# Optimization experiments

Hardware: AMD Instinct MI355X
Metric: run time of the kernel (lower is better)

## Reference

```python
import math
import jax, jax.numpy as jnp
import numpy as np

HEAD_NUM = 8
DIM = 512
D_K = DIM // HEAD_NUM  # 64
M_FEAT = 256
B, L = 4, 2048
STAB = 1e-5


def _orthogonal_gaussian(m, d, rng):
    num_squares = m // d
    blocks = []
    for _ in range(num_squares):
        q, _ = np.linalg.qr(rng.standard_normal((d, d)))
        blocks.append(q.T)
    rem = m - d * num_squares
    if rem:
        q, _ = np.linalg.qr(rng.standard_normal((d, d)))
        blocks.append(q.T[:rem])
    mat = np.concatenate(blocks, axis=0)
    mat = mat / math.sqrt(num_squares + rem / d)
    return mat.astype(np.float32)


def setup_inputs() -> dict:
    key = jax.random.key(0)
    ks = jax.random.split(key, 12)
    rng = np.random.default_rng(0)
    inp = {
        'query': jax.random.normal(ks[0], (B, L, DIM), jnp.float32),
        'key': jax.random.normal(ks[1], (B, L, DIM), jnp.float32),
        'value': jax.random.normal(ks[2], (B, L, DIM), jnp.float32),
        'proj': jnp.asarray(_orthogonal_gaussian(M_FEAT, D_K, rng)),  # [M, d_k]
        'w_q_w': jax.random.normal(ks[3], (DIM, DIM), jnp.float32) * 0.02,
        'w_q_b': jnp.zeros((DIM,), jnp.float32),
        'w_k_w': jax.random.normal(ks[4], (DIM, DIM), jnp.float32) * 0.02,
        'w_k_b': jnp.zeros((DIM,), jnp.float32),
        'w_v_w': jax.random.normal(ks[5], (DIM, DIM), jnp.float32) * 0.02,
        'w_v_b': jnp.zeros((DIM,), jnp.float32),
        'w_o_w': jax.random.normal(ks[6], (DIM, DIM), jnp.float32) * 0.02,
        'w_o_b': jnp.zeros((DIM,), jnp.float32),
    }
    return inp


def _relu_kernel(data, proj):
    # data: [B,L,H,D], proj: [M,D] -> [B,L,H,M]
    ratio = 1.0 / math.sqrt(proj.shape[0])
    return jax.nn.relu(ratio * jnp.einsum('blhd,md->blhm', data, proj)) + STAB


def _favor_causal(qp, kp, vs):
    # qp, kp: [L,B,H,M]; vs: [L,B,H,D] -> num [L,B,H,D], den [L,B,H]
    b, h, m = qp.shape[1], qp.shape[2], qp.shape[3]
    d = vs.shape[3]
    carry0 = (jnp.zeros((b, h, m, d), qp.dtype), jnp.zeros((b, h, m), qp.dtype))

    def step(carry, inp):
        s_kv, s_k = carry
        q_l, k_l, v_l = inp
        s_kv = s_kv + jnp.einsum('bhm,bhd->bhmd', k_l, v_l)
        s_k = s_k + k_l
        num = jnp.einsum('bhmd,bhm->bhd', s_kv, q_l)
        den = jnp.sum(q_l * s_k, axis=-1)
        return (s_kv, s_k), (num, den)

    _, (num, den) = jax.lax.scan(step, carry0, (qp, kp, vs))
    return num, den


def reference(query, key, value, proj, w_q_w, w_q_b, w_k_w, w_k_b, w_v_w, w_v_b, w_o_w, w_o_b):
    bsz = query.shape[0]
    q = (query @ w_q_w.T + w_q_b).reshape(bsz, -1, HEAD_NUM, D_K)
    k = (key @ w_k_w.T + w_k_b).reshape(bsz, -1, HEAD_NUM, D_K)
    v = (value @ w_v_w.T + w_v_b).reshape(bsz, -1, HEAD_NUM, D_K)
    qp = jnp.swapaxes(_relu_kernel(q, proj), 0, 1)  # [L,B,H,M]
    kp = jnp.swapaxes(_relu_kernel(k, proj), 0, 1)
    vs = jnp.swapaxes(v, 0, 1)                      # [L,B,H,D]
    num, den = _favor_causal(qp, kp, vs)
    attn = jnp.swapaxes(num, 0, 1) / jnp.swapaxes(den, 0, 1)[..., None]  # [B,L,H,D]
    attn = attn.reshape(bsz, -1, HEAD_NUM * D_K)
    return attn @ w_o_w.T + w_o_b
```

## Files before the change

kernel.cpp:

```cpp
#include <hip/hip_runtime.h>
#include <stdint.h>

#define B_ 4
#define L_ 2048
#define H_ 8
#define DK 64
#define M_ 256
#define DIM_ 512
#define NTOK (B_ * L_)
#define CHK 128
#define NC (L_ / CHK)
#define BH (B_ * H_)
#define RATIO 0.0625f
#define STABC 1e-5f

typedef unsigned short ushort_t;
typedef __attribute__((ext_vector_type(8))) short bf8v;
typedef __attribute__((ext_vector_type(4))) float f4v;

#define MFMA16(a, b, c) __builtin_amdgcn_mfma_f32_16x16x32_bf16(a, b, c, 0, 0, 0)

__device__ __forceinline__ ushort_t f2bf(float f) {
  uint32_t u = __float_as_uint(f);
  return (ushort_t)((u + 0x7fffu + ((u >> 16) & 1u)) >> 16);
}
__device__ __forceinline__ float bf2f(ushort_t u) { return __uint_as_float(((uint32_t)u) << 16); }

__device__ __forceinline__ void gll16(const void* g, void* l) {
  __builtin_amdgcn_global_load_lds((const __attribute__((address_space(1))) void*)g,
                                   (__attribute__((address_space(3))) void*)l, 16, 0, 0);
}

__device__ __forceinline__ bf8v ldfrag(const ushort_t* base, int row, int cb) {
  return *(const bf8v*)((const char*)base + row * 128 + (cb ^ ((row & 7) << 4)));
}
__device__ __forceinline__ bf8v ldfrag256(const ushort_t* base, int row, int cb) {
  return *(const bf8v*)((const char*)base + row * 256 + (cb ^ ((row & 7) << 4)));
}
__device__ __forceinline__ bf8v ldfrag512(const ushort_t* base, int row, int cb) {
  return *(const bf8v*)((const char*)base + row * 512 + (cb ^ ((row & 7) << 4)));
}

__global__ __launch_bounds__(256) void cvt_w(const float* __restrict__ wq, const float* __restrict__ wk,
                                             const float* __restrict__ wv, const float* __restrict__ wo,
                                             const float* __restrict__ pj, ushort_t* __restrict__ d) {
  int i = (blockIdx.x * 256 + threadIdx.x) * 8;
  const float* s;
  int off;
  if (i < 262144)       { s = wq; off = i; }
  else if (i < 524288)  { s = wk; off = i - 262144; }
  else if (i < 786432)  { s = wv; off = i - 524288; }
  else if (i < 1048576) { s = wo; off = i - 786432; }
  else                  { s = pj; off = i - 1048576; }
  float4 a = *(const float4*)(s + off);
  float4 b = *(const float4*)(s + off + 4);
  union { ushort_t u[8]; uint4 vv; } o;
  o.u[0] = f2bf(a.x); o.u[1] = f2bf(a.y); o.u[2] = f2bf(a.z); o.u[3] = f2bf(a.w);
  o.u[4] = f2bf(b.x); o.u[5] = f2bf(b.y); o.u[6] = f2bf(b.z); o.u[7] = f2bf(b.w);
  *(uint4*)(d + i) = o.vv;
}

__global__ __launch_bounds__(256) void qkvgemm_k(const float* __restrict__ q, const float* __restrict__ k,
                                                 const float* __restrict__ v, const ushort_t* __restrict__ Wc,
                                                 const float* __restrict__ bq, const float* __restrict__ bk,
                                                 const float* __restrict__ bv, ushort_t* __restrict__ XHq,
                                                 ushort_t* __restrict__ XHk, ushort_t* __restrict__ VT) {
  __shared__ char SB[65536];
  ushort_t* Tt = (ushort_t*)SB;
  const int z = blockIdx.z;
  const float* X = (z == 0) ? q : (z == 1) ? k : v;
  const ushort_t* Bw = Wc + (size_t)z * 262144;
  const float* bias = (z == 0) ? bq : (z == 1) ? bk : bv;
  const int tid = threadIdx.x, lane = tid & 63, w = tid >> 6;
  const int bm = blockIdx.x * 128, bn = blockIdx.y * 128;
  const int srow = w * 8 + (lane >> 3);
  const int scol = (((lane & 7) * 16) ^ ((lane >> 3) << 4)) >> 1;
  const int wr = (w >> 1) * 64, wc = (w & 1) * 64;
  const int fr = lane & 15, ks = lane >> 4, fq = lane >> 4;
  f4v acc[4][4] = {};
  {
#pragma unroll
    for (int i = 0; i < 4; ++i)
      gll16(Bw + (size_t)(bn + i * 32 + srow) * DIM_ + scol, SB + 32768 + i * 4096 + w * 1024);
#pragma unroll
    for (int i = 0; i < 4; ++i) {
      int e = tid + i * 256;
      int r = e >> 3, g = e & 7;
      const float* src = X + (size_t)(bm + r) * DIM_ + g * 8;
      float4 f0 = *(const float4*)src;
      float4 f1 = *(const float4*)(src + 4);
      union { ushort_t u[8]; bf8v v8; } pk;
      pk.u[0] = f2bf(f0.x); pk.u[1] = f2bf(f0.y); pk.u[2] = f2bf(f0.z); pk.u[3] = f2bf(f0.w);
      pk.u[4] = f2bf(f1.x); pk.u[5] = f2bf(f1.y); pk.u[6] = f2bf(f1.z); pk.u[7] = f2bf(f1.w);
      *(bf8v*)(SB + r * 128 + ((g * 16) ^ ((r & 7) << 4))) = pk.v8;
    }
  }
  __syncthreads();
  for (int t = 0; t < 8; ++t) {
    const ushort_t* curA = (const ushort_t*)(SB + (t & 1) * 16384);
    const ushort_t* curB = (const ushort_t*)(SB + 32768 + (t & 1) * 16384);
    char* nxtA = SB + ((t + 1) & 1) * 16384;
    char* nxtB = SB + 32768 + ((t + 1) & 1) * 16384;
    const int nk = (t + 1) * 64;
    float4 fA[4][2];
    if (t < 7) {
#pragma unroll
      for (int i = 0; i < 4; ++i) {
        int e = tid + i * 256;
        int r = e >> 3, g = e & 7;
        const float* src = X + (size_t)(bm + r) * DIM_ + nk + g * 8;
        fA[i][0] = *(const float4*)src;
        fA[i][1] = *(const float4*)(src + 4);
      }
#pragma unroll
      for (int i = 0; i < 4; ++i)
        gll16(Bw + (size_t)(bn + i * 32 + srow) * DIM_ + nk + scol, nxtB + i * 4096 + w * 1024);
    }
#pragma unroll
    for (int kk = 0; kk < 2; ++kk) {
      const int cb = kk * 64 + ks * 16;
      bf8v av[4], bv2[4];
#pragma unroll
      for (int m = 0; m < 4; ++m) av[m] = ldfrag(curA, wr + m * 16 + fr, cb);
#pragma unroll
      for (int n = 0; n < 4; ++n) bv2[n] = ldfrag(curB, wc + n * 16 + fr, cb);
#pragma unroll
      for (int m = 0; m < 4; ++m)
#pragma unroll
        for (int n = 0; n < 4; ++n) acc[m][n] = MFMA16(av[m], bv2[n], acc[m][n]);
    }
    if (t < 7) {
#pragma unroll
      for (int i = 0; i < 4; ++i) {
        int e = tid + i * 256;
        int r = e >> 3, g = e & 7;
        union { ushort_t u[8]; bf8v v8; } pk;
        pk.u[0] = f2bf(fA[i][0].x); pk.u[1] = f2bf(fA[i][0].y);
        pk.u[2] = f2bf(fA[i][0].z); pk.u[3] = f2bf(fA[i][0].w);
        pk.u[4] = f2bf(fA[i][1].x); pk.u[5] = f2bf(fA[i][1].y);
        pk.u[6] = f2bf(fA[i][1].z); pk.u[7] = f2bf(fA[i][1].w);
        *(bf8v*)(nxtA + r * 128 + ((g * 16) ^ ((r & 7) << 4))) = pk.v8;
      }
    }
    __syncthreads();
  }
  if (z == 2) {
#pragma unroll
    for (int m = 0; m < 4; ++m)
#pragma unroll
      for (int n = 0; n < 4; ++n) {
        int cl = wc + n * 16 + fr;
        float bsv = bias[bn + cl];
#pragma unroll
        for (int j = 0; j < 4; ++j) {
          int rl = wr + m * 16 + fq * 4 + j;
          Tt[cl * 136 + rl] = f2bf(acc[m][n][j] + bsv);
        }
      }
    __syncthreads();
    const int dl = tid >> 1, seg = tid & 1;
    const int c = bn + dl;
    const int bh2 = (bm >> 11) * 8 + (c >> 6);
    const int drow = c & 63;
    size_t vbase = ((size_t)(bh2 * 64 + drow)) * L_ + (bm & 2047) + seg * 64;
#pragma unroll
    for (int qq = 0; qq < 8; ++qq)
      *(uint4*)&VT[vbase + qq * 8] = *(const uint4*)&Tt[dl * 136 + seg * 64 + qq * 8];
  } else {
    ushort_t* Y = (z == 0) ? XHq : XHk;
#pragma unroll
    for (int m = 0; m < 4; ++m)
#pragma unroll
      for (int n = 0; n < 4; ++n) {
        int col = bn + wc + n * 16 + fr;
        float bsv = bias[col];
#pragma unroll
        for (int j = 0; j < 4; ++j) {
          int row = bm + wr + m * 16 + fq * 4 + j;
          Y[(size_t)row * DIM_ + col] = f2bf(acc[m][n][j] + bsv);
        }
      }
  }
}

__global__ __launch_bounds__(256) void cp2_k(const ushort_t* __restrict__ XHk, const ushort_t* __restrict__ P,
                                             const ushort_t* __restrict__ VT, ushort_t* __restrict__ kp,
                                             ushort_t* __restrict__ S) {
  __shared__ ushort_t Ps[256 * 64];
  __shared__ ushort_t Xs[128 * 64];
  __shared__ ushort_t Kt[256 * 128];
  const int ci = blockIdx.x, bh = blockIdx.y;
  const int b = bh >> 3, h = bh & 7;
  const int tid = threadIdx.x, lane = tid & 63, w = tid >> 6;
  const int srow = w * 8 + (lane >> 3);
  const int scol = (((lane & 7) * 16) ^ ((lane >> 3) << 4)) >> 1;
  const int fr = lane & 15, ks = lane >> 4, fq = lane >> 4;
  const int l0 = ci * CHK;
#pragma unroll
  for (int i = 0; i < 8; ++i)
    gll16(P + (size_t)(i * 32 + srow) * 64 + scol, (char*)Ps + i * 4096 + w * 1024);
#pragma unroll
  for (int i = 0; i < 4; ++i)
    gll16(XHk + (size_t)(b * L_ + l0 + i * 32 + srow) * DIM_ + h * 64 + scol, (char*)Xs + i * 4096 + w * 1024);
  __syncthreads();
  {
    f4v acc[4][8] = {};
#pragma unroll
    for (int kk = 0; kk < 2; ++kk) {
      const int cb = kk * 64 + ks * 16;
      bf8v av[4], bv[8];
#pragma unroll
      for (int m = 0; m < 4; ++m) av[m] = ldfrag(Ps, w * 64 + m * 16 + fr, cb);
#pragma unroll
      for (int n = 0; n < 8; ++n) bv[n] = ldfrag(Xs, n * 16 + fr, cb);
#pragma unroll
      for (int m = 0; m < 4; ++m)
#pragma unroll
        for (int n = 0; n < 8; ++n) acc[m][n] = MFMA16(av[m], bv[n], acc[m][n]);
    }
#pragma unroll
    for (int m = 0; m < 4; ++m)
#pragma unroll
      for (int n = 0; n < 8; ++n) {
        const int mb = w * 64 + m * 16 + fq * 4;
        const int ll = n * 16 + fr;
        ushort_t bvv[4];
#pragma unroll
        for (int j = 0; j < 4; ++j) {
          float v = fmaxf(RATIO * acc[m][n][j], 0.f) + STABC;
          bvv[j] = f2bf(v);
          *(ushort_t*)((char*)Kt + (mb + j) * 256 + ((ll * 2) ^ (((mb + j) & 7) << 4))) = bvv[j];
        }
        uint2 pk;
        pk.x = (uint32_t)bvv[0] | ((uint32_t)bvv[1] << 16);
        pk.y = (uint32_t)bvv[2] | ((uint32_t)bvv[3] << 16);
        *(uint2*)(kp + ((size_t)bh * L_ + l0 + ll) * M_ + mb) = pk;
      }
  }
  __syncthreads();
  f4v accS[5][4] = {};
  for (int kt = 0; kt < 2; ++kt) {
#pragma unroll
    for (int i = 0; i < 2; ++i)
      gll16(VT + ((size_t)bh * 64 + i * 32 + srow) * L_ + l0 + kt * 64 + scol, (char*)Xs + i * 4096 + w * 1024);
    if (tid < 32) ((uint32_t*)Xs)[2048 + tid] = 0x3f803f80u;
    __syncthreads();
#pragma unroll
    for (int kk = 0; kk < 2; ++kk) {
      const int cbA = kk * 64 + ks * 16;
      const int cbK = kt * 128 + kk * 64 + ks * 16;
      bf8v av[5], bv[4];
#pragma unroll
      for (int a = 0; a < 5; ++a) av[a] = ldfrag(Xs, a * 16 + fr, cbA);
#pragma unroll
      for (int n = 0; n < 4; ++n) bv[n] = ldfrag256(Kt, w * 64 + n * 16 + fr, cbK);
#pragma unroll
      for (int a = 0; a < 5; ++a)
#pragma unroll
        for (int n = 0; n < 4; ++n) accS[a][n] = MFMA16(av[a], bv[n], accS[a][n]);
    }
    __syncthreads();
  }
  const size_t base = ((size_t)bh * NC + ci) * 65;
#pragma unroll
  for (int a = 0; a < 5; ++a)
#pragma unroll
    for (int n = 0; n < 4; ++n)
#pragma unroll
      for (int j = 0; j < 4; ++j) {
        int row = a * 16 + fq * 4 + j;
        if (row < 65) S[(base + row) * M_ + w * 64 + n * 16 + fr] = f2bf(accS[a][n][j]);
      }
}

__global__ __launch_bounds__(256) void prefix2_k(ushort_t* __restrict__ S) {
  const int g = blockIdx.x * 256 + threadIdx.x;
  const int bh = g / 2080, r = g - bh * 2080;
  ushort_t* base = S + (size_t)bh * (NC * 65 * M_) + (size_t)r * 8;
  uint4 v[16];
#pragma unroll
  for (int ci = 0; ci < NC; ++ci) v[ci] = *(const uint4*)(base + (size_t)ci * (65 * M_));
  float c[8] = {};
#pragma unroll
  for (int ci = 0; ci < NC; ++ci) {
    union { uint4 u; ushort_t s[8]; } in, out;
    in.u = v[ci];
#pragma unroll
    for (int e = 0; e < 8; ++e) {
      float t = bf2f(in.s[e]);
      out.s[e] = f2bf(c[e]);
      c[e] += t;
    }
    *(uint4*)(base + (size_t)ci * (65 * M_)) = out.u;
  }
}

__global__ __launch_bounds__(512) void qkout3_k(const ushort_t* __restrict__ XHq, const ushort_t* __restrict__ P,
                                                const ushort_t* __restrict__ kp, const ushort_t* __restrict__ VT,
                                                const ushort_t* __restrict__ S, ushort_t* __restrict__ attn) {
  __shared__ char LB[114688];
  ushort_t* Qp = (ushort_t*)LB;
  ushort_t* R1 = (ushort_t*)(LB + 65536);
  ushort_t* R2 = (ushort_t*)(LB + 98304);
  const int ci = blockIdx.x, bh = blockIdx.y;
  const int b = bh >> 3, h = bh & 7;
  const int tid = threadIdx.x, lane = tid & 63, w = tid >> 6;
  const int srow = w * 8 + (lane >> 3);
  const int scol = (((lane & 7) * 16) ^ ((lane >> 3) << 4)) >> 1;
  const int fr = lane & 15, ks = lane >> 4, fq = lane >> 4;
  const int l0 = ci * CHK;
  const size_t rowb = (size_t)bh * L_ + l0;
  const size_t tokb = (size_t)b * L_ + l0;
  const size_t sbase = ((size_t)bh * NC + ci) * 65;
#pragma unroll
  for (int i = 0; i < 4; ++i)
    gll16(P + (size_t)(i * 64 + srow) * 64 + scol, (char*)R1 + i * 8192 + w * 1024);
#pragma unroll
  for (int i = 0; i < 2; ++i)
    gll16(XHq + (tokb + i * 64 + srow) * DIM_ + h * 64 + scol, (char*)R2 + i * 8192 + w * 1024);
  __syncthreads();
  {
    f4v accF[2][8] = {};
#pragma unroll
    for (int kk = 0; kk < 2; ++kk) {
      const int cb = kk * 64 + ks * 16;
      bf8v av[2], bv[8];
#pragma unroll
      for (int m = 0; m < 2; ++m) av[m] = ldfrag(R1, w * 32 + m * 16 + fr, cb);
#pragma unroll
      for (int n = 0; n < 8; ++n) bv[n] = ldfrag(R2, n * 16 + fr, cb);
#pragma unroll
      for (int m = 0; m < 2; ++m)
#pragma unroll
        for (int n = 0; n < 8; ++n) accF[m][n] = MFMA16(av[m], bv[n], accF[m][n]);
    }
#pragma unroll
    for (int m = 0; m < 2; ++m)
#pragma unroll
      for (int n = 0; n < 8; ++n) {
        const int mb = w * 32 + m * 16 + fq * 4;
        const int ll = n * 16 + fr;
        ushort_t bvv[4];
#pragma unroll
        for (int j = 0; j < 4; ++j)
          bvv[j] = f2bf(fmaxf(RATIO * accF[m][n][j], 0.f) + STABC);
        uint2 pk;
        pk.x = (uint32_t)bvv[0] | ((uint32_t)bvv[1] << 16);
        pk.y = (uint32_t)bvv[2] | ((uint32_t)bvv[3] << 16);
        *(uint2*)((char*)Qp + ll * 512 + ((mb * 2) ^ ((ll & 7) << 4))) = pk;
      }
  }
  __syncthreads();
  const int qr = (w & 3) * 32, qc = (w >> 2) * 64;
  const int orow = w * 16;
  f4v accA[2][4] = {};
  f4v acc2[5] = {};
  for (int kt = 0; kt < 4; ++kt) {
#pragma unroll
    for (int i = 0; i < 2; ++i)
      gll16(kp + (rowb + i * 64 + srow) * M_ + kt * 64 + scol, (char*)R1 + i * 8192 + w * 1024);
    gll16(S + (sbase + srow) * M_ + kt * 64 + scol, (char*)R2 + w * 1024);
    if (tid < 32)
      ((uint32_t*)R2)[2048 + tid] = ((const uint32_t*)(S + (sbase + 64) * M_ + kt * 64))[tid];
    __syncthreads();
#pragma unroll
    for (int kk = 0; kk < 2; ++kk) {
      const int cb = kk * 64 + ks * 16;
      const int cbQ = kt * 128 + cb;
      bf8v aq[2], bk_[4], a2, sv[5];
#pragma unroll
      for (int m = 0; m < 2; ++m) aq[m] = ldfrag512(Qp, qr + m * 16 + fr, cbQ);
#pragma unroll
      for (int n = 0; n < 4; ++n) bk_[n] = ldfrag(R1, qc + n * 16 + fr, cb);
#pragma unroll
      for (int m = 0; m < 2; ++m)
#pragma unroll
        for (int n = 0; n < 4; ++n) accA[m][n] = MFMA16(aq[m], bk_[n], accA[m][n]);
      a2 = ldfrag512(Qp, orow + fr, cbQ);
#pragma unroll
      for (int n = 0; n < 5; ++n) sv[n] = ldfrag(R2, n * 16 + fr, cb);
#pragma unroll
      for (int n = 0; n < 5; ++n) acc2[n] = MFMA16(a2, sv[n], acc2[n]);
    }
    __syncthreads();
  }
#pragma unroll
  for (int m = 0; m < 2; ++m)
#pragma unroll
    for (int n = 0; n < 4; ++n)
#pragma unroll
      for (int j = 0; j < 4; ++j) {
        int row = qr + m * 16 + fq * 4 + j;
        int col = qc + n * 16 + fr;
        float v = (col <= row) ? accA[m][n][j] : 0.f;
        *(ushort_t*)((char*)R1 + row * 256 + ((col * 2) ^ ((row & 7) << 4))) = f2bf(v);
      }
  __syncthreads();
  for (int kt2 = 0; kt2 < 2; ++kt2) {
    gll16(VT + ((size_t)bh * 64 + srow) * L_ + l0 + kt2 * 64 + scol, (char*)R2 + w * 1024);
    if (tid < 32) ((uint32_t*)R2)[2048 + tid] = 0x3f803f80u;
    __syncthreads();
#pragma unroll
    for (int kk = 0; kk < 2; ++kk) {
      const int cb = kk * 64 + ks * 16;
      bf8v a3, sv[5];
      a3 = ldfrag256(R1, orow + fr, kt2 * 128 + cb);
#pragma unroll
      for (int n = 0; n < 5; ++n) sv[n] = ldfrag(R2, n * 16 + fr, cb);
#pragma unroll
      for (int n = 0; n < 5; ++n) acc2[n] = MFMA16(a3, sv[n], acc2[n]);
    }
    __syncthreads();
  }
  float dinv[4];
#pragma unroll
  for (int j = 0; j < 4; ++j) {
    float den = __shfl(acc2[4][j], (lane & 48));
    dinv[j] = 1.f / den;
  }
#pragma unroll
  for (int n = 0; n < 4; ++n)
#pragma unroll
    for (int j = 0; j < 4; ++j) {
      int l = orow + fq * 4 + j;
      int col = h * 64 + n * 16 + fr;
      attn[(tokb + l) * DIM_ + col] = f2bf(acc2[n][j] * dinv[j]);
    }
}

__global__ __launch_bounds__(256) void gemmo_k(const ushort_t* __restrict__ A, const ushort_t* __restrict__ Bw,
                                               const float* __restrict__ bias, float* __restrict__ Y) {
  __shared__ char SB[49152];
  const int tid = threadIdx.x, lane = tid & 63, w = tid >> 6;
  const int bm = blockIdx.x * 128, bn = blockIdx.y * 64;
  const int srow = w * 8 + (lane >> 3);
  const int scol = (((lane & 7) * 16) ^ ((lane >> 3) << 4)) >> 1;
  const int wr = (w >> 1) * 64, wc = (w & 1) * 32;
  const int fr = lane & 15, ks = lane >> 4, fq = lane >> 4;
  f4v acc[4][2] = {};
#pragma unroll
  for (int i = 0; i < 4; ++i)
    gll16(A + (size_t)(bm + i * 32 + srow) * DIM_ + scol, SB + i * 4096 + w * 1024);
#pragma unroll
  for (int i = 0; i < 2; ++i)
    gll16(Bw + (size_t)(bn + i * 32 + srow) * DIM_ + scol, SB + 32768 + i * 4096 + w * 1024);
  __syncthreads();
  for (int t = 0; t < 8; ++t) {
    const ushort_t* curA = (const ushort_t*)(SB + (t & 1) * 16384);
    const ushort_t* curB = (const ushort_t*)(SB + 32768 + (t & 1) * 8192);
    char* nxtA = SB + ((t + 1) & 1) * 16384;
    char* nxtB = SB + 32768 + ((t + 1) & 1) * 8192;
    const int nk = (t + 1) * 64;
    if (t < 7) {
#pragma unroll
      for (int i = 0; i < 4; ++i)
        gll16(A + (size_t)(bm + i * 32 + srow) * DIM_ + nk + scol, nxtA + i * 4096 + w * 1024);
#pragma unroll
      for (int i = 0; i < 2; ++i)
        gll16(Bw + (size_t)(bn + i * 32 + srow) * DIM_ + nk + scol, nxtB + i * 4096 + w * 1024);
    }
#pragma unroll
    for (int kk = 0; kk < 2; ++kk) {
      const int cb = kk * 64 + ks * 16;
      bf8v av[4], bv[2];
#pragma unroll
      for (int m = 0; m < 4; ++m) av[m] = ldfrag(curA, wr + m * 16 + fr, cb);
#pragma unroll
      for (int n = 0; n < 2; ++n) bv[n] = ldfrag(curB, wc + n * 16 + fr, cb);
#pragma unroll
      for (int m = 0; m < 4; ++m)
#pragma unroll
        for (int n = 0; n < 2; ++n) acc[m][n] = MFMA16(av[m], bv[n], acc[m][n]);
    }
    __syncthreads();
  }
#pragma unroll
  for (int m = 0; m < 4; ++m)
#pragma unroll
    for (int n = 0; n < 2; ++n) {
      int col = bn + wc + n * 16 + fr;
      float bsv = bias[col];
#pragma unroll
      for (int j = 0; j < 4; ++j) {
        int row = bm + wr + m * 16 + fq * 4 + j;
        Y[(size_t)row * DIM_ + col] = acc[m][n][j] + bsv;
      }
    }
}

extern "C" void kernel_launch(void* const* d_in, const int* in_sizes, int n_in,
                              void* d_out, int out_size, void* d_ws, size_t ws_size,
                              hipStream_t stream) {
  const float* query = (const float*)d_in[0];
  const float* key   = (const float*)d_in[1];
  const float* value = (const float*)d_in[2];
  const float* proj  = (const float*)d_in[3];
  const float* wq = (const float*)d_in[4];
  const float* bq = (const float*)d_in[5];
  const float* wk = (const float*)d_in[6];
  const float* bk = (const float*)d_in[7];
  const float* wv = (const float*)d_in[8];
  const float* bv = (const float*)d_in[9];
  const float* wo = (const float*)d_in[10];
  const float* bo = (const float*)d_in[11];

  char* ws = (char*)d_ws;
  ushort_t* Wc   = (ushort_t*)(ws);
  ushort_t* XHq  = (ushort_t*)(ws + 2129920);
  ushort_t* XHk  = (ushort_t*)(ws + 10518528);
  ushort_t* VT   = (ushort_t*)(ws + 18907136);
  ushort_t* kp   = (ushort_t*)(ws + 27295744);
  ushort_t* Skv  = (ushort_t*)(ws + 60850176);
  ushort_t* attb = (ushort_t*)(ws + 77889536);
  const ushort_t* Wo = Wc + 786432;
  const ushort_t* Pc = Wc + 1048576;

  dim3 blk(256);
  cvt_w<<<520, blk, 0, stream>>>(wq, wk, wv, wo, proj, Wc);
  qkvgemm_k<<<dim3(64, 4, 3), blk, 0, stream>>>(query, key, value, Wc, bq, bk, bv, XHq, XHk, VT);
  cp2_k<<<dim3(NC, BH), blk, 0, stream>>>(XHk, Pc, VT, kp, Skv);
  prefix2_k<<<260, blk, 0, stream>>>(Skv);
  qkout3_k<<<dim3(NC, BH), dim3(512), 0, stream>>>(XHq, Pc, kp, VT, Skv, attb);
  gemmo_k<<<dim3(64, 8), blk, 0, stream>>>(attb, Wo, bo, (float*)d_out);
}
```

Measured before the change: 100.3 us.

## Recompute key features in output kernel instead of storing kp; remap QKV GEMM blocks to XCDs

The cp2 kernel no longer writes the key random-feature tensor (kp, about 33MB in bf16) to global memory. The output kernel instead loads the raw key head slice and recomputes the ReLU feature tiles per k-chunk with extra MFMAs into a new LDS region. This raises LDS use to 144KB. Separately, the QKV GEMM now remaps its flat block index so blocks sharing the same X rows land on the same XCD, which should improve L2 reuse. The trade is avoided global write and read traffic in exchange for duplicated feature computation and larger LDS per block.

Result: no change. 99.23 us (-1.1%).

```diff
diff --git a/kernel.cpp b/kernel.cpp
--- a/kernel.cpp
+++ b/kernel.cpp
@@ -67,12 +67,16 @@
                                                  ushort_t* __restrict__ XHk, ushort_t* __restrict__ VT) {
   __shared__ char SB[65536];
   ushort_t* Tt = (ushort_t*)SB;
-  const int z = blockIdx.z;
+  const int flat = blockIdx.x + (blockIdx.y << 6) + (blockIdx.z << 8);
+  const int xcd = flat & 7, sl = flat >> 3;
+  const int p = sl >> 2, bnn = sl & 3;
+  const int idx = xcd * 24 + p;
+  const int z = idx >> 6;
+  const int bm = (idx & 63) * 128, bn = bnn * 128;
   const float* X = (z == 0) ? q : (z == 1) ? k : v;
   const ushort_t* Bw = Wc + (size_t)z * 262144;
   const float* bias = (z == 0) ? bq : (z == 1) ? bk : bv;
   const int tid = threadIdx.x, lane = tid & 63, w = tid >> 6;
-  const int bm = blockIdx.x * 128, bn = blockIdx.y * 128;
   const int srow = w * 8 + (lane >> 3);
   const int scol = (((lane & 7) * 16) ^ ((lane >> 3) << 4)) >> 1;
   const int wr = (w >> 1) * 64, wc = (w & 1) * 64;
@@ -184,8 +188,7 @@
 }
 
 __global__ __launch_bounds__(256) void cp2_k(const ushort_t* __restrict__ XHk, const ushort_t* __restrict__ P,
-                                             const ushort_t* __restrict__ VT, ushort_t* __restrict__ kp,
-                                             ushort_t* __restrict__ S) {
+                                             const ushort_t* __restrict__ VT, ushort_t* __restrict__ S) {
   __shared__ ushort_t Ps[256 * 64];
   __shared__ ushort_t Xs[128 * 64];
   __shared__ ushort_t Kt[256 * 128];
@@ -224,17 +227,11 @@
       for (int n = 0; n < 8; ++n) {
         const int mb = w * 64 + m * 16 + fq * 4;
         const int ll = n * 16 + fr;
-        ushort_t bvv[4];
 #pragma unroll
         for (int j = 0; j < 4; ++j) {
           float v = fmaxf(RATIO * acc[m][n][j], 0.f) + STABC;
-          bvv[j] = f2bf(v);
-          *(ushort_t*)((char*)Kt + (mb + j) * 256 + ((ll * 2) ^ (((mb + j) & 7) << 4))) = bvv[j];
+          *(ushort_t*)((char*)Kt + (mb + j) * 256 + ((ll * 2) ^ (((mb + j) & 7) << 4))) = f2bf(v);
         }
-        uint2 pk;
-        pk.x = (uint32_t)bvv[0] | ((uint32_t)bvv[1] << 16);
-        pk.y = (uint32_t)bvv[2] | ((uint32_t)bvv[3] << 16);
-        *(uint2*)(kp + ((size_t)bh * L_ + l0 + ll) * M_ + mb) = pk;
       }
   }
   __syncthreads();
@@ -295,13 +292,15 @@
   }
 }
 
-__global__ __launch_bounds__(512) void qkout3_k(const ushort_t* __restrict__ XHq, const ushort_t* __restrict__ P,
-                                                const ushort_t* __restrict__ kp, const ushort_t* __restrict__ VT,
+__global__ __launch_bounds__(512) void qkout4_k(const ushort_t* __restrict__ XHq, const ushort_t* __restrict__ XHk,
+                                                const ushort_t* __restrict__ P, const ushort_t* __restrict__ VT,
                                                 const ushort_t* __restrict__ S, ushort_t* __restrict__ attn) {
-  __shared__ char LB[114688];
-  ushort_t* Qp = (ushort_t*)LB;
-  ushort_t* R1 = (ushort_t*)(LB + 65536);
-  ushort_t* R2 = (ushort_t*)(LB + 98304);
+  __shared__ char LB[147456];
+  ushort_t* Qp  = (ushort_t*)LB;
+  ushort_t* Pj  = (ushort_t*)(LB + 65536);
+  ushort_t* Kps = (ushort_t*)(LB + 98304);
+  ushort_t* R2  = (ushort_t*)(LB + 114688);
+  ushort_t* Xk  = (ushort_t*)(LB + 131072);
   const int ci = blockIdx.x, bh = blockIdx.y;
   const int b = bh >> 3, h = bh & 7;
   const int tid = threadIdx.x, lane = tid & 63, w = tid >> 6;
@@ -309,15 +308,16 @@
   const int scol = (((lane & 7) * 16) ^ ((lane >> 3) << 4)) >> 1;
   const int fr = lane & 15, ks = lane >> 4, fq = lane >> 4;
   const int l0 = ci * CHK;
-  const size_t rowb = (size_t)bh * L_ + l0;
   const size_t tokb = (size_t)b * L_ + l0;
   const size_t sbase = ((size_t)bh * NC + ci) * 65;
 #pragma unroll
   for (int i = 0; i < 4; ++i)
-    gll16(P + (size_t)(i * 64 + srow) * 64 + scol, (char*)R1 + i * 8192 + w * 1024);
-#pragma unroll
-  for (int i = 0; i < 2; ++i)
+    gll16(P + (size_t)(i * 64 + srow) * 64 + scol, (char*)Pj + i * 8192 + w * 1024);
+#pragma unroll
+  for (int i = 0; i < 2; ++i) {
     gll16(XHq + (tokb + i * 64 + srow) * DIM_ + h * 64 + scol, (char*)R2 + i * 8192 + w * 1024);
+    gll16(XHk + (tokb + i * 64 + srow) * DIM_ + h * 64 + scol, (char*)Xk + i * 8192 + w * 1024);
+  }
   __syncthreads();
   {
     f4v accF[2][8] = {};
@@ -326,7 +326,7 @@
       const int cb = kk * 64 + ks * 16;
       bf8v av[2], bv[8];
 #pragma unroll
-      for (int m = 0; m < 2; ++m) av[m] = ldfrag(R1, w * 32 + m * 16 + fr, cb);
+      for (int m = 0; m < 2; ++m) av[m] = ldfrag(Pj, w * 32 + m * 16 + fr, cb);
 #pragma unroll
       for (int n = 0; n < 8; ++n) bv[n] = ldfrag(R2, n * 16 + fr, cb);
 #pragma unroll
@@ -356,12 +356,33 @@
   f4v accA[2][4] = {};
   f4v acc2[5] = {};
   for (int kt = 0; kt < 4; ++kt) {
-#pragma unroll
-    for (int i = 0; i < 2; ++i)
-      gll16(kp + (rowb + i * 64 + srow) * M_ + kt * 64 + scol, (char*)R1 + i * 8192 + w * 1024);
     gll16(S + (sbase + srow) * M_ + kt * 64 + scol, (char*)R2 + w * 1024);
     if (tid < 32)
       ((uint32_t*)R2)[2048 + tid] = ((const uint32_t*)(S + (sbase + 64) * M_ + kt * 64))[tid];
+    {
+      const int fi = w >> 1, tf0 = (w & 1) * 4;
+      f4v accK[4] = {};
+#pragma unroll
+      for (int kk = 0; kk < 2; ++kk) {
+        const int cb = kk * 64 + ks * 16;
+        bf8v ap = ldfrag(Pj, kt * 64 + fi * 16 + fr, cb);
+        bf8v bx[4];
+#pragma unroll
+        for (int t2 = 0; t2 < 4; ++t2) bx[t2] = ldfrag(Xk, (tf0 + t2) * 16 + fr, cb);
+#pragma unroll
+        for (int t2 = 0; t2 < 4; ++t2) accK[t2] = MFMA16(ap, bx[t2], accK[t2]);
+      }
+#pragma unroll
+      for (int t2 = 0; t2 < 4; ++t2) {
+        const int tt = (tf0 + t2) * 16 + fr;
+        const int fl = fi * 16 + fq * 4;
+#pragma unroll
+        for (int j = 0; j < 4; ++j) {
+          float v = fmaxf(RATIO * accK[t2][j], 0.f) + STABC;
+          *(ushort_t*)((char*)Kps + tt * 128 + (((fl + j) * 2) ^ ((tt & 7) << 4))) = f2bf(v);
+        }
+      }
+    }
     __syncthreads();
 #pragma unroll
     for (int kk = 0; kk < 2; ++kk) {
@@ -371,7 +392,7 @@
 #pragma unroll
       for (int m = 0; m < 2; ++m) aq[m] = ldfrag512(Qp, qr + m * 16 + fr, cbQ);
 #pragma unroll
-      for (int n = 0; n < 4; ++n) bk_[n] = ldfrag(R1, qc + n * 16 + fr, cb);
+      for (int n = 0; n < 4; ++n) bk_[n] = ldfrag(Kps, qc + n * 16 + fr, cb);
 #pragma unroll
       for (int m = 0; m < 2; ++m)
 #pragma unroll
@@ -393,7 +414,7 @@
         int row = qr + m * 16 + fq * 4 + j;
         int col = qc + n * 16 + fr;
         float v = (col <= row) ? accA[m][n][j] : 0.f;
-        *(ushort_t*)((char*)R1 + row * 256 + ((col * 2) ^ ((row & 7) << 4))) = f2bf(v);
+        *(ushort_t*)((char*)Pj + row * 256 + ((col * 2) ^ ((row & 7) << 4))) = f2bf(v);
       }
   __syncthreads();
   for (int kt2 = 0; kt2 < 2; ++kt2) {
@@ -404,7 +425,7 @@
     for (int kk = 0; kk < 2; ++kk) {
       const int cb = kk * 64 + ks * 16;
       bf8v a3, sv[5];
-      a3 = ldfrag256(R1, orow + fr, kt2 * 128 + cb);
+      a3 = ldfrag256(Pj, orow + fr, kt2 * 128 + cb);
 #pragma unroll
       for (int n = 0; n < 5; ++n) sv[n] = ldfrag(R2, n * 16 + fr, cb);
 #pragma unroll
@@ -509,17 +530,16 @@
   ushort_t* XHq  = (ushort_t*)(ws + 2129920);
   ushort_t* XHk  = (ushort_t*)(ws + 10518528);
   ushort_t* VT   = (ushort_t*)(ws + 18907136);
-  ushort_t* kp   = (ushort_t*)(ws + 27295744);
-  ushort_t* Skv  = (ushort_t*)(ws + 60850176);
-  ushort_t* attb = (ushort_t*)(ws + 77889536);
+  ushort_t* Skv  = (ushort_t*)(ws + 27295744);
+  ushort_t* attb = (ushort_t*)(ws + 44335104);
   const ushort_t* Wo = Wc + 786432;
   const ushort_t* Pc = Wc + 1048576;
 
   dim3 blk(256);
   cvt_w<<<520, blk, 0, stream>>>(wq, wk, wv, wo, proj, Wc);
   qkvgemm_k<<<dim3(64, 4, 3), blk, 0, stream>>>(query, key, value, Wc, bq, bk, bv, XHq, XHk, VT);
-  cp2_k<<<dim3(NC, BH), blk, 0, stream>>>(XHk, Pc, VT, kp, Skv);
+  cp2_k<<<dim3(NC, BH), blk, 0, stream>>>(XHk, Pc, VT, Skv);
   prefix2_k<<<260, blk, 0, stream>>>(Skv);
-  qkout3_k<<<dim3(NC, BH), dim3(512), 0, stream>>>(XHq, Pc, kp, VT, Skv, attb);
+  qkout4_k<<<dim3(NC, BH), dim3(512), 0, stream>>>(XHq, XHk, Pc, VT, Skv, attb);
   gemmo_k<<<dim3(64, 8), blk, 0, stream>>>(attb, Wo, bo, (float*)d_out);
 }
```
